# Performance work log

Measured on AMD Instinct MI355X. Metric: run time of the kernel, lower is better.

The kernel has to match this reference:

```python
import jax, jax.numpy as jnp
import numpy as np

D = 1024
HEADS = 16
HEAD_DIM = D // HEADS
B = 4
L = 1024


def setup_inputs() -> dict:
    key = jax.random.key(0)
    kq, kk, kv, kw, kb = jax.random.split(key, 5)
    Q = jax.random.normal(kq, (B, L, D), dtype=jnp.float32)
    K = jax.random.normal(kk, (B, L, D), dtype=jnp.float32)
    V = jax.random.normal(kv, (B, L, D), dtype=jnp.float32)
    # Output projection H: torch nn.Linear(D, D) -> weight (D, D), bias (D,)
    lim = 1.0 / np.sqrt(D)
    W_H = jax.random.uniform(kw, (D, D), minval=-lim, maxval=lim, dtype=jnp.float32)
    b_H = jax.random.uniform(kb, (D,), minval=-lim, maxval=lim, dtype=jnp.float32)
    mask = 0  # falsy -> no masking branch, matching `if mask` in the source
    return {"Q": Q, "K": K, "V": V, "W_H": W_H, "b_H": b_H, "mask": mask}


def reference(Q, K, V, W_H, b_H, mask):
    batch, q_len, _ = Q.shape
    k_len = K.shape[1]
    Qh = Q.reshape(batch, q_len, HEADS, HEAD_DIM)
    Kh = K.reshape(batch, k_len, HEADS, HEAD_DIM)
    Vh = V.reshape(batch, k_len, HEADS, HEAD_DIM)
    scores = jnp.einsum('bqhd,bkhd->bhqk', Qh, Kh)  # [B,H,Lq,Lk]
    if mask:  # mask is a Python scalar (0 -> skip), as in source
        scores = jnp.where(mask == 0, -jnp.inf, scores)
    # NOTE: source scales by sqrt(D), not sqrt(head_dim)
    attn = jax.nn.softmax(scores / np.sqrt(D).astype(np.float32), axis=3)
    out = jnp.einsum('bhql,blhd->bqhd', attn, Vh).reshape(batch, q_len, D)
    return out @ W_H.T + b_H
```

## Files before the change

kernel.cpp:

```cpp
#include <hip/hip_runtime.h>
#include <hip/hip_bf16.h>

typedef __attribute__((ext_vector_type(4))) float f32x4;
typedef __attribute__((ext_vector_type(8))) short bf16x8;
typedef __attribute__((ext_vector_type(4))) short bf16x4;

#if __has_builtin(__builtin_amdgcn_mfma_f32_16x16x16_bf16)
#define MFMA_16x16x16(a, b, c) __builtin_amdgcn_mfma_f32_16x16x16_bf16(a, b, c, 0, 0, 0)
#else
#define MFMA_16x16x16(a, b, c) __builtin_amdgcn_mfma_f32_16x16x16bf16_1k(a, b, c, 0, 0, 0)
#endif

constexpr int Bn  = 4;
constexpr int Ln  = 1024;
constexpr int Dn  = 1024;
constexpr int Hn  = 16;
constexpr int HDn = 64;

static __device__ __forceinline__ unsigned short bf16r(float f) {
    union { float f; unsigned int u; } x;
    x.f = f;
    unsigned int r = x.u + 0x7fffu + ((x.u >> 16) & 1u);
    return (unsigned short)(r >> 16);
}

__global__ __launch_bounds__(256) void prep_kernel(
    const float* __restrict__ Kg, const float* __restrict__ Vg,
    const float* __restrict__ Wg, unsigned short* __restrict__ Kbf,
    unsigned short* __restrict__ Vtg, unsigned short* __restrict__ Wbf)
{
    const int tid = threadIdx.x;
    if (blockIdx.z == 4) {
        const int r0 = blockIdx.x * 64, c0 = blockIdx.y * 64;
        for (int i = 0; i < 4; ++i) {
            int e4 = i * 256 + tid;
            int r = e4 >> 4, c4 = e4 & 15;
            float4 v = *(const float4*)(Wg + (size_t)(r0 + r) * Dn + c0 + c4 * 4);
            ushort4 o;
            o.x = bf16r(v.x); o.y = bf16r(v.y); o.z = bf16r(v.z); o.w = bf16r(v.w);
            *(ushort4*)(Wbf + (size_t)(r0 + r) * Dn + c0 + c4 * 4) = o;
        }
        return;
    }

    __shared__ unsigned short T[64][72];
    const int k0 = blockIdx.x * 64;
    const int h  = blockIdx.y;
    const int b  = blockIdx.z;
    const float* Kb = Kg + (size_t)b * Ln * Dn + h * HDn;
    const float* Vb = Vg + (size_t)b * Ln * Dn + h * HDn;
    unsigned short* Ko = Kbf + (size_t)b * Ln * Dn + h * HDn;

    for (int i = 0; i < 4; ++i) {
        int e4 = i * 256 + tid;
        int r = e4 >> 4, c4 = e4 & 15;
        float4 kv = *(const float4*)(Kb + (size_t)(k0 + r) * Dn + c4 * 4);
        ushort4 o;
        o.x = bf16r(kv.x); o.y = bf16r(kv.y); o.z = bf16r(kv.z); o.w = bf16r(kv.w);
        *(ushort4*)(Ko + (size_t)(k0 + r) * Dn + c4 * 4) = o;
        float4 vv = *(const float4*)(Vb + (size_t)(k0 + r) * Dn + c4 * 4);
        T[c4 * 4 + 0][r] = bf16r(vv.x);
        T[c4 * 4 + 1][r] = bf16r(vv.y);
        T[c4 * 4 + 2][r] = bf16r(vv.z);
        T[c4 * 4 + 3][r] = bf16r(vv.w);
    }
    __syncthreads();
    unsigned short* out = Vtg + ((size_t)(b * Hn + h) * HDn) * Ln + k0;
    for (int i = 0; i < 2; ++i) {
        int e8 = i * 256 + tid;
        int r = e8 >> 3, c8 = e8 & 7;
        *(uint4*)(out + (size_t)r * Ln + c8 * 8) = *(const uint4*)&T[r][c8 * 8];
    }
}

__global__ __launch_bounds__(512) void attn_kernel(
    const float* __restrict__ Qg, const unsigned short* __restrict__ Kbf,
    const unsigned short* __restrict__ Vtg, unsigned short* __restrict__ Xg)
{
    __shared__ unsigned short Ks[64][72];
    __shared__ unsigned short Vts[64][72];

    const int tid  = threadIdx.x;
    const int wave = tid >> 6;
    const int lane = tid & 63;
    const int l16  = lane & 15;
    const int quad = lane >> 4;

    const int h  = blockIdx.x;
    const int q0 = blockIdx.y * 128;
    const int b  = blockIdx.z;

    const unsigned short* Kb16 = Kbf + (size_t)b * Ln * Dn + h * HDn;
    const unsigned short* Vtb  = Vtg + ((size_t)(b * Hn + h) * HDn) * Ln;

    bf16x8 aq0, aq1;
    {
        const float* qp = Qg + ((size_t)b * Ln + q0 + wave * 16 + l16) * Dn
                             + h * HDn + quad * 8;
        float4 a0 = *(const float4*)qp;
        float4 a1 = *(const float4*)(qp + 4);
        float4 a2 = *(const float4*)(qp + 32);
        float4 a3 = *(const float4*)(qp + 36);
        aq0[0] = (short)bf16r(a0.x); aq0[1] = (short)bf16r(a0.y);
        aq0[2] = (short)bf16r(a0.z); aq0[3] = (short)bf16r(a0.w);
        aq0[4] = (short)bf16r(a1.x); aq0[5] = (short)bf16r(a1.y);
        aq0[6] = (short)bf16r(a1.z); aq0[7] = (short)bf16r(a1.w);
        aq1[0] = (short)bf16r(a2.x); aq1[1] = (short)bf16r(a2.y);
        aq1[2] = (short)bf16r(a2.z); aq1[3] = (short)bf16r(a2.w);
        aq1[4] = (short)bf16r(a3.x); aq1[5] = (short)bf16r(a3.y);
        aq1[6] = (short)bf16r(a3.z); aq1[7] = (short)bf16r(a3.w);
    }

    const float SC = 1.4426950408889634f / 32.0f;

    float lsum = 0.f;
    f32x4 Oacc[4];
    for (int d = 0; d < 4; ++d) Oacc[d] = (f32x4){0.f, 0.f, 0.f, 0.f};

    for (int it = 0; it < Ln / 64; ++it) {
        const int k0 = it * 64;
        __syncthreads();
        {
            int r = tid >> 3, c8 = tid & 7;
            *(uint4*)&Ks[r][c8 * 8] =
                *(const uint4*)(Kb16 + (size_t)(k0 + r) * Dn + c8 * 8);
            *(uint4*)&Vts[r][c8 * 8] =
                *(const uint4*)(Vtb + (size_t)r * Ln + k0 + c8 * 8);
        }
        __syncthreads();

        f32x4 s[4];
        for (int n = 0; n < 4; ++n) {
            bf16x8 ka0 = *(const bf16x8*)&Ks[n * 16 + l16][quad * 8];
            bf16x8 ka1 = *(const bf16x8*)&Ks[n * 16 + l16][32 + quad * 8];
            f32x4 acc = (f32x4){0.f, 0.f, 0.f, 0.f};
            acc = __builtin_amdgcn_mfma_f32_16x16x32_bf16(ka0, aq0, acc, 0, 0, 0);
            acc = __builtin_amdgcn_mfma_f32_16x16x32_bf16(ka1, aq1, acc, 0, 0, 0);
            s[n] = acc;
        }

        bf16x4 pf[4];
        for (int n = 0; n < 4; ++n) {
            float p0 = exp2f(s[n][0] * SC);
            float p1 = exp2f(s[n][1] * SC);
            float p2 = exp2f(s[n][2] * SC);
            float p3 = exp2f(s[n][3] * SC);
            lsum += (p0 + p1) + (p2 + p3);
            unsigned int u0 = __float_as_uint(p0) + 0x8000u;
            unsigned int u1 = __float_as_uint(p1) + 0x8000u;
            unsigned int u2 = __float_as_uint(p2) + 0x8000u;
            unsigned int u3 = __float_as_uint(p3) + 0x8000u;
            union { unsigned int u[2]; bf16x4 v; } pk;
            pk.u[0] = __builtin_amdgcn_perm(u1, u0, 0x07060302u);
            pk.u[1] = __builtin_amdgcn_perm(u3, u2, 0x07060302u);
            pf[n] = pk.v;
        }

        for (int dt = 0; dt < 4; ++dt)
            for (int kn = 0; kn < 4; ++kn) {
                bf16x4 bv = *(const bf16x4*)&Vts[dt * 16 + l16][kn * 16 + quad * 4];
                Oacc[dt] = MFMA_16x16x16(pf[kn], bv, Oacc[dt]);
            }
    }

    lsum += __shfl_xor(lsum, 16, 64);
    lsum += __shfl_xor(lsum, 32, 64);
    float linv[4];
    for (int r = 0; r < 4; ++r)
        linv[r] = 1.f / __shfl(lsum, quad * 4 + r, 64);

    unsigned short* Xb = Xg + ((size_t)b * Ln + q0) * Dn + h * HDn;
    for (int r = 0; r < 4; ++r) {
        int row = wave * 16 + quad * 4 + r;
        for (int d = 0; d < 4; ++d)
            Xb[(size_t)row * Dn + d * 16 + l16] = bf16r(Oacc[d][r] * linv[r]);
    }
}

__global__ __launch_bounds__(512) void proj_kernel(
    const unsigned short* __restrict__ Xg, const unsigned short* __restrict__ Wbf,
    const float* __restrict__ bg, float* __restrict__ Yg)
{
    __shared__ unsigned short Xs[128][72];
    __shared__ unsigned short Wsh[128][72];

    const int tid  = threadIdx.x;
    const int wave = tid >> 6;
    const int lane = tid & 63;
    const int l16  = lane & 15;
    const int quad = lane >> 4;
    const int mw   = (wave & 1) * 64;
    const int nw   = (wave >> 1) * 32;

    const int n0 = blockIdx.x * 128;
    const int m0 = blockIdx.y * 128;

    f32x4 acc[4][2];
    for (int mt = 0; mt < 4; ++mt)
        for (int nt = 0; nt < 2; ++nt)
            acc[mt][nt] = (f32x4){0.f, 0.f, 0.f, 0.f};

    for (int it = 0; it < Dn / 64; ++it) {
        const int kk0 = it * 64;
        __syncthreads();
        {
            int r = tid >> 3, c8 = tid & 7;
            const unsigned short* xp = Xg + (size_t)(m0 + r) * Dn + kk0 + c8 * 8;
            *(uint4*)&Xs[r][c8 * 8]      = *(const uint4*)xp;
            *(uint4*)&Xs[r + 64][c8 * 8] = *(const uint4*)(xp + (size_t)64 * Dn);
            const unsigned short* wp = Wbf + (size_t)(n0 + r) * Dn + kk0 + c8 * 8;
            *(uint4*)&Wsh[r][c8 * 8]      = *(const uint4*)wp;
            *(uint4*)&Wsh[r + 64][c8 * 8] = *(const uint4*)(wp + (size_t)64 * Dn);
        }
        __syncthreads();

        bf16x8 af[4][2], bfr[2][2];
        for (int mt = 0; mt < 4; ++mt)
            for (int kk = 0; kk < 2; ++kk)
                af[mt][kk] = *(const bf16x8*)&Xs[mw + mt * 16 + l16][kk * 32 + quad * 8];
        for (int nt = 0; nt < 2; ++nt)
            for (int kk = 0; kk < 2; ++kk)
                bfr[nt][kk] = *(const bf16x8*)&Wsh[nw + nt * 16 + l16][kk * 32 + quad * 8];
        for (int mt = 0; mt < 4; ++mt)
            for (int nt = 0; nt < 2; ++nt) {
                acc[mt][nt] = __builtin_amdgcn_mfma_f32_16x16x32_bf16(
                    af[mt][0], bfr[nt][0], acc[mt][nt], 0, 0, 0);
                acc[mt][nt] = __builtin_amdgcn_mfma_f32_16x16x32_bf16(
                    af[mt][1], bfr[nt][1], acc[mt][nt], 0, 0, 0);
            }
    }

    for (int nt = 0; nt < 2; ++nt) {
        int col = n0 + nw + nt * 16 + l16;
        float bb = bg[col];
        for (int mt = 0; mt < 4; ++mt)
            for (int r = 0; r < 4; ++r) {
                int row = m0 + mw + mt * 16 + quad * 4 + r;
                Yg[(size_t)row * Dn + col] = acc[mt][nt][r] + bb;
            }
    }
}

extern "C" void kernel_launch(void* const* d_in, const int* in_sizes, int n_in,
                              void* d_out, int out_size, void* d_ws, size_t ws_size,
                              hipStream_t stream) {
    const float* Q    = (const float*)d_in[0];
    const float* K    = (const float*)d_in[1];
    const float* V    = (const float*)d_in[2];
    const float* W    = (const float*)d_in[3];
    const float* bias = (const float*)d_in[4];

    unsigned short* Kbf = (unsigned short*)d_ws;
    unsigned short* Vt  = Kbf + (size_t)Bn * Ln * Dn;
    unsigned short* Wbf = Vt  + (size_t)Bn * Ln * Dn;
    unsigned short* X   = Wbf + (size_t)Dn * Dn;
    float* Y = (float*)d_out;

    dim3 gp(Ln / 64, Hn, Bn + 1);
    prep_kernel<<<gp, 256, 0, stream>>>(K, V, W, Kbf, Vt, Wbf);

    dim3 g1(Hn, Ln / 128, Bn);
    attn_kernel<<<g1, 512, 0, stream>>>(Q, Kbf, Vt, X);

    dim3 g2(Dn / 128, (Bn * Ln) / 128);
    proj_kernel<<<g2, 512, 0, stream>>>(X, Wbf, bias, Y);
}
```

Baseline: 157.1 us.

## Prepack V into MFMA fragment order and give each attention wave two query tiles

The prep kernel now writes transposed V in per-segment MFMA fragment order, so the attention kernel copies it into LDS contiguously and each lane reads one bf16x4 directly. Attention blocks shrink to 4 waves, each handling 32 query rows (two 16-row sets), so every K and V fragment loaded from LDS feeds two MFMAs. The projection kernel moves to 256 threads with a 64-wide N tile, which doubles the grid. The changes aim to cut LDS traffic and bank conflicts per MFMA, at the cost of more registers per wave and fewer waves per block for hiding latency.

```diff
diff --git a/kernel.cpp b/kernel.cpp
--- a/kernel.cpp
+++ b/kernel.cpp
@@ -16,6 +16,8 @@
 constexpr int Dn  = 1024;
 constexpr int Hn  = 16;
 constexpr int HDn = 64;
+constexpr int SEGS = Ln / 64;
+constexpr int SEG_SHORTS = 16 * 64 * 4;
 
 static __device__ __forceinline__ unsigned short bf16r(float f) {
     union { float f; unsigned int u; } x;
@@ -44,9 +46,10 @@
     }
 
     __shared__ unsigned short T[64][72];
-    const int k0 = blockIdx.x * 64;
-    const int h  = blockIdx.y;
-    const int b  = blockIdx.z;
+    const int seg = blockIdx.x;
+    const int k0  = seg * 64;
+    const int h   = blockIdx.y;
+    const int b   = blockIdx.z;
     const float* Kb = Kg + (size_t)b * Ln * Dn + h * HDn;
     const float* Vb = Vg + (size_t)b * Ln * Dn + h * HDn;
     unsigned short* Ko = Kbf + (size_t)b * Ln * Dn + h * HDn;
@@ -65,20 +68,27 @@
         T[c4 * 4 + 3][r] = bf16r(vv.w);
     }
     __syncthreads();
-    unsigned short* out = Vtg + ((size_t)(b * Hn + h) * HDn) * Ln + k0;
+
+    unsigned short* out = Vtg + ((size_t)(b * Hn + h) * SEGS + seg) * SEG_SHORTS;
     for (int i = 0; i < 2; ++i) {
-        int e8 = i * 256 + tid;
-        int r = e8 >> 3, c8 = e8 & 7;
-        *(uint4*)(out + (size_t)r * Ln + c8 * 8) = *(const uint4*)&T[r][c8 * 8];
-    }
-}
-
-__global__ __launch_bounds__(512) void attn_kernel(
+        int g = i * 256 + tid;
+        int fid = g >> 5, a = g & 31;
+        int kn = fid >> 2, dt = fid & 3;
+        int L0 = 2 * a, L1 = 2 * a + 1;
+        ushort4 lo = *(const ushort4*)&T[dt * 16 + (L0 & 15)][kn * 16 + (L0 >> 4) * 4];
+        ushort4 hi = *(const ushort4*)&T[dt * 16 + (L1 & 15)][kn * 16 + (L1 >> 4) * 4];
+        union { ushort4 s[2]; uint4 u; } pk;
+        pk.s[0] = lo; pk.s[1] = hi;
+        *(uint4*)(out + (size_t)g * 8) = pk.u;
+    }
+}
+
+__global__ __launch_bounds__(256) void attn_kernel(
     const float* __restrict__ Qg, const unsigned short* __restrict__ Kbf,
     const unsigned short* __restrict__ Vtg, unsigned short* __restrict__ Xg)
 {
     __shared__ unsigned short Ks[64][72];
-    __shared__ unsigned short Vts[64][72];
+    __shared__ unsigned short Vf[SEG_SHORTS];
 
     const int tid  = threadIdx.x;
     const int wave = tid >> 6;
@@ -91,98 +101,116 @@
     const int b  = blockIdx.z;
 
     const unsigned short* Kb16 = Kbf + (size_t)b * Ln * Dn + h * HDn;
-    const unsigned short* Vtb  = Vtg + ((size_t)(b * Hn + h) * HDn) * Ln;
-
-    bf16x8 aq0, aq1;
-    {
-        const float* qp = Qg + ((size_t)b * Ln + q0 + wave * 16 + l16) * Dn
+    const unsigned short* Vsegs = Vtg + ((size_t)(b * Hn + h) * SEGS) * SEG_SHORTS;
+
+    bf16x8 aq[2][2];
+    for (int set = 0; set < 2; ++set) {
+        const float* qp = Qg + ((size_t)b * Ln + q0 + wave * 32 + set * 16 + l16) * Dn
                              + h * HDn + quad * 8;
         float4 a0 = *(const float4*)qp;
         float4 a1 = *(const float4*)(qp + 4);
         float4 a2 = *(const float4*)(qp + 32);
         float4 a3 = *(const float4*)(qp + 36);
-        aq0[0] = (short)bf16r(a0.x); aq0[1] = (short)bf16r(a0.y);
-        aq0[2] = (short)bf16r(a0.z); aq0[3] = (short)bf16r(a0.w);
-        aq0[4] = (short)bf16r(a1.x); aq0[5] = (short)bf16r(a1.y);
-        aq0[6] = (short)bf16r(a1.z); aq0[7] = (short)bf16r(a1.w);
-        aq1[0] = (short)bf16r(a2.x); aq1[1] = (short)bf16r(a2.y);
-        aq1[2] = (short)bf16r(a2.z); aq1[3] = (short)bf16r(a2.w);
-        aq1[4] = (short)bf16r(a3.x); aq1[5] = (short)bf16r(a3.y);
-        aq1[6] = (short)bf16r(a3.z); aq1[7] = (short)bf16r(a3.w);
+        bf16x8 q0v, q1v;
+        q0v[0] = (short)bf16r(a0.x); q0v[1] = (short)bf16r(a0.y);
+        q0v[2] = (short)bf16r(a0.z); q0v[3] = (short)bf16r(a0.w);
+        q0v[4] = (short)bf16r(a1.x); q0v[5] = (short)bf16r(a1.y);
+        q0v[6] = (short)bf16r(a1.z); q0v[7] = (short)bf16r(a1.w);
+        q1v[0] = (short)bf16r(a2.x); q1v[1] = (short)bf16r(a2.y);
+        q1v[2] = (short)bf16r(a2.z); q1v[3] = (short)bf16r(a2.w);
+        q1v[4] = (short)bf16r(a3.x); q1v[5] = (short)bf16r(a3.y);
+        q1v[6] = (short)bf16r(a3.z); q1v[7] = (short)bf16r(a3.w);
+        aq[set][0] = q0v; aq[set][1] = q1v;
     }
 
     const float SC = 1.4426950408889634f / 32.0f;
 
-    float lsum = 0.f;
-    f32x4 Oacc[4];
-    for (int d = 0; d < 4; ++d) Oacc[d] = (f32x4){0.f, 0.f, 0.f, 0.f};
-
-    for (int it = 0; it < Ln / 64; ++it) {
+    float lsum[2] = {0.f, 0.f};
+    f32x4 Oacc[2][4];
+    for (int s = 0; s < 2; ++s)
+        for (int d = 0; d < 4; ++d) Oacc[s][d] = (f32x4){0.f, 0.f, 0.f, 0.f};
+
+    for (int it = 0; it < SEGS; ++it) {
         const int k0 = it * 64;
         __syncthreads();
         {
-            int r = tid >> 3, c8 = tid & 7;
-            *(uint4*)&Ks[r][c8 * 8] =
-                *(const uint4*)(Kb16 + (size_t)(k0 + r) * Dn + c8 * 8);
-            *(uint4*)&Vts[r][c8 * 8] =
-                *(const uint4*)(Vtb + (size_t)r * Ln + k0 + c8 * 8);
+            for (int i = 0; i < 2; ++i) {
+                int s = i * 256 + tid;
+                int r = s >> 3, c8 = s & 7;
+                *(uint4*)&Ks[r][c8 * 8] =
+                    *(const uint4*)(Kb16 + (size_t)(k0 + r) * Dn + c8 * 8);
+            }
+            const unsigned short* vsrc = Vsegs + (size_t)it * SEG_SHORTS;
+            for (int i = 0; i < 2; ++i) {
+                int s = i * 256 + tid;
+                *(uint4*)&Vf[s * 8] = *(const uint4*)(vsrc + (size_t)s * 8);
+            }
         }
         __syncthreads();
 
-        f32x4 s[4];
+        f32x4 st[2][4];
         for (int n = 0; n < 4; ++n) {
             bf16x8 ka0 = *(const bf16x8*)&Ks[n * 16 + l16][quad * 8];
             bf16x8 ka1 = *(const bf16x8*)&Ks[n * 16 + l16][32 + quad * 8];
-            f32x4 acc = (f32x4){0.f, 0.f, 0.f, 0.f};
-            acc = __builtin_amdgcn_mfma_f32_16x16x32_bf16(ka0, aq0, acc, 0, 0, 0);
-            acc = __builtin_amdgcn_mfma_f32_16x16x32_bf16(ka1, aq1, acc, 0, 0, 0);
-            s[n] = acc;
-        }
-
-        bf16x4 pf[4];
-        for (int n = 0; n < 4; ++n) {
-            float p0 = exp2f(s[n][0] * SC);
-            float p1 = exp2f(s[n][1] * SC);
-            float p2 = exp2f(s[n][2] * SC);
-            float p3 = exp2f(s[n][3] * SC);
-            lsum += (p0 + p1) + (p2 + p3);
-            unsigned int u0 = __float_as_uint(p0) + 0x8000u;
-            unsigned int u1 = __float_as_uint(p1) + 0x8000u;
-            unsigned int u2 = __float_as_uint(p2) + 0x8000u;
-            unsigned int u3 = __float_as_uint(p3) + 0x8000u;
-            union { unsigned int u[2]; bf16x4 v; } pk;
-            pk.u[0] = __builtin_amdgcn_perm(u1, u0, 0x07060302u);
-            pk.u[1] = __builtin_amdgcn_perm(u3, u2, 0x07060302u);
-            pf[n] = pk.v;
-        }
+            for (int set = 0; set < 2; ++set) {
+                f32x4 acc = (f32x4){0.f, 0.f, 0.f, 0.f};
+                acc = __builtin_amdgcn_mfma_f32_16x16x32_bf16(ka0, aq[set][0], acc, 0, 0, 0);
+                acc = __builtin_amdgcn_mfma_f32_16x16x32_bf16(ka1, aq[set][1], acc, 0, 0, 0);
+                st[set][n] = acc;
+            }
+        }
+
+        bf16x4 pf[2][4];
+        for (int set = 0; set < 2; ++set)
+            for (int n = 0; n < 4; ++n) {
+                float p0 = exp2f(st[set][n][0] * SC);
+                float p1 = exp2f(st[set][n][1] * SC);
+                float p2 = exp2f(st[set][n][2] * SC);
+                float p3 = exp2f(st[set][n][3] * SC);
+                lsum[set] += (p0 + p1) + (p2 + p3);
+                unsigned int u0 = __float_as_uint(p0) + 0x8000u;
+                unsigned int u1 = __float_as_uint(p1) + 0x8000u;
+                unsigned int u2 = __float_as_uint(p2) + 0x8000u;
+                unsigned int u3 = __float_as_uint(p3) + 0x8000u;
+                union { unsigned int u[2]; bf16x4 v; } pk;
+                pk.u[0] = __builtin_amdgcn_perm(u1, u0, 0x07060302u);
+                pk.u[1] = __builtin_amdgcn_perm(u3, u2, 0x07060302u);
+                pf[set][n] = pk.v;
+            }
 
         for (int dt = 0; dt < 4; ++dt)
             for (int kn = 0; kn < 4; ++kn) {
-                bf16x4 bv = *(const bf16x4*)&Vts[dt * 16 + l16][kn * 16 + quad * 4];
-                Oacc[dt] = MFMA_16x16x16(pf[kn], bv, Oacc[dt]);
-            }
-    }
-
-    lsum += __shfl_xor(lsum, 16, 64);
-    lsum += __shfl_xor(lsum, 32, 64);
-    float linv[4];
-    for (int r = 0; r < 4; ++r)
-        linv[r] = 1.f / __shfl(lsum, quad * 4 + r, 64);
+                bf16x4 bv = *(const bf16x4*)&Vf[((kn * 4 + dt) * 64 + lane) * 4];
+                Oacc[0][dt] = MFMA_16x16x16(pf[0][kn], bv, Oacc[0][dt]);
+                Oacc[1][dt] = MFMA_16x16x16(pf[1][kn], bv, Oacc[1][dt]);
+            }
+    }
+
+    float linv[2][4];
+    for (int set = 0; set < 2; ++set) {
+        float rs = lsum[set];
+        rs += __shfl_xor(rs, 16, 64);
+        rs += __shfl_xor(rs, 32, 64);
+        for (int r = 0; r < 4; ++r)
+            linv[set][r] = 1.f / __shfl(rs, quad * 4 + r, 64);
+    }
 
     unsigned short* Xb = Xg + ((size_t)b * Ln + q0) * Dn + h * HDn;
-    for (int r = 0; r < 4; ++r) {
-        int row = wave * 16 + quad * 4 + r;
-        for (int d = 0; d < 4; ++d)
-            Xb[(size_t)row * Dn + d * 16 + l16] = bf16r(Oacc[d][r] * linv[r]);
-    }
-}
-
-__global__ __launch_bounds__(512) void proj_kernel(
+    for (int set = 0; set < 2; ++set)
+        for (int r = 0; r < 4; ++r) {
+            int row = wave * 32 + set * 16 + quad * 4 + r;
+            for (int dt = 0; dt < 4; ++dt)
+                Xb[(size_t)row * Dn + dt * 16 + l16] =
+                    bf16r(Oacc[set][dt][r] * linv[set][r]);
+        }
+}
+
+__global__ __launch_bounds__(256) void proj_kernel(
     const unsigned short* __restrict__ Xg, const unsigned short* __restrict__ Wbf,
     const float* __restrict__ bg, float* __restrict__ Yg)
 {
     __shared__ unsigned short Xs[128][72];
-    __shared__ unsigned short Wsh[128][72];
+    __shared__ unsigned short Wsh[64][72];
 
     const int tid  = threadIdx.x;
     const int wave = tid >> 6;
@@ -192,7 +220,7 @@
     const int mw   = (wave & 1) * 64;
     const int nw   = (wave >> 1) * 32;
 
-    const int n0 = blockIdx.x * 128;
+    const int n0 = blockIdx.x * 64;
     const int m0 = blockIdx.y * 128;
 
     f32x4 acc[4][2];
@@ -204,13 +232,18 @@
         const int kk0 = it * 64;
         __syncthreads();
         {
-            int r = tid >> 3, c8 = tid & 7;
-            const unsigned short* xp = Xg + (size_t)(m0 + r) * Dn + kk0 + c8 * 8;
-            *(uint4*)&Xs[r][c8 * 8]      = *(const uint4*)xp;
-            *(uint4*)&Xs[r + 64][c8 * 8] = *(const uint4*)(xp + (size_t)64 * Dn);
-            const unsigned short* wp = Wbf + (size_t)(n0 + r) * Dn + kk0 + c8 * 8;
-            *(uint4*)&Wsh[r][c8 * 8]      = *(const uint4*)wp;
-            *(uint4*)&Wsh[r + 64][c8 * 8] = *(const uint4*)(wp + (size_t)64 * Dn);
+            for (int i = 0; i < 4; ++i) {
+                int s = i * 256 + tid;
+                int r = s >> 3, c8 = s & 7;
+                *(uint4*)&Xs[r][c8 * 8] =
+                    *(const uint4*)(Xg + (size_t)(m0 + r) * Dn + kk0 + c8 * 8);
+            }
+            for (int i = 0; i < 2; ++i) {
+                int s = i * 256 + tid;
+                int r = s >> 3, c8 = s & 7;
+                *(uint4*)&Wsh[r][c8 * 8] =
+                    *(const uint4*)(Wbf + (size_t)(n0 + r) * Dn + kk0 + c8 * 8);
+            }
         }
         __syncthreads();
 
@@ -256,12 +289,12 @@
     unsigned short* X   = Wbf + (size_t)Dn * Dn;
     float* Y = (float*)d_out;
 
-    dim3 gp(Ln / 64, Hn, Bn + 1);
+    dim3 gp(SEGS, Hn, Bn + 1);
     prep_kernel<<<gp, 256, 0, stream>>>(K, V, W, Kbf, Vt, Wbf);
 
     dim3 g1(Hn, Ln / 128, Bn);
-    attn_kernel<<<g1, 512, 0, stream>>>(Q, Kbf, Vt, X);
-
-    dim3 g2(Dn / 128, (Bn * Ln) / 128);
-    proj_kernel<<<g2, 512, 0, stream>>>(X, Wbf, bias, Y);
-}
+    attn_kernel<<<g1, 256, 0, stream>>>(Q, Kbf, Vt, X);
+
+    dim3 g2(Dn / 64, (Bn * Ln) / 128);
+    proj_kernel<<<g2, 256, 0, stream>>>(X, Wbf, bias, Y);
+}
```

After: 164.5 us. +4.7%, slower.
